# Kernel tuning notes

Hardware: AMD Instinct MI355X
Metric: run time of the kernel (lower is better)

## Reference

```python
import jax, jax.numpy as jnp
import numpy as np

DIM = 4096
N_HEADS = 32
N_KV = 8
HEAD_DIM = DIM // N_HEADS  # 128
R = N_HEADS // N_KV        # 4 query heads per kv head
B, T = 2, 2048


def setup_inputs() -> dict:
    key = jax.random.key(0)
    kx, kq, kkv, ko = jax.random.split(key, 4)
    scale = 0.02
    return {
        "x": jax.random.normal(kx, (B, T, DIM), dtype=jnp.float32),
        "Wq": jax.random.normal(kq, (DIM, DIM), dtype=jnp.float32) * scale,
        "Wkv": jax.random.normal(kkv, (2 * N_KV * HEAD_DIM, DIM), dtype=jnp.float32) * scale,
        "Wo": jax.random.normal(ko, (DIM, DIM), dtype=jnp.float32) * scale,
    }


def reference(x, Wq, Wkv, Wo):
    Bs, Ts, C = x.shape
    # projections (torch Linear: y = x @ W.T)
    q = (x @ Wq.T).reshape(Bs, Ts, N_HEADS, HEAD_DIM).transpose(0, 2, 1, 3)  # [B,H,T,hd]
    kv = x @ Wkv.T                                                            # [B,T,2*KV*hd]
    k, v = jnp.split(kv, 2, axis=-1)
    k = k.reshape(Bs, Ts, N_KV, HEAD_DIM).transpose(0, 2, 1, 3)  # [B,KV,T,hd]
    v = v.reshape(Bs, Ts, N_KV, HEAD_DIM).transpose(0, 2, 1, 3)  # [B,KV,T,hd]
    # grouped query heads: head h = g*R + r matches repeat_interleave(R, dim=1)
    qg = q.reshape(Bs, N_KV, R, Ts, HEAD_DIM)                    # [B,KV,R,T,hd]
    inv_scale = 1.0 / np.sqrt(HEAD_DIM).astype(np.float32)
    scores = jnp.einsum("bgrtd,bgsd->bgrts", qg, k) * inv_scale  # [B,KV,R,T,T]
    causal = jnp.tril(jnp.ones((Ts, Ts), dtype=bool))
    scores = jnp.where(causal, scores, jnp.finfo(scores.dtype).min)
    attn = jax.nn.softmax(scores, axis=-1)
    o = jnp.einsum("bgrts,bgsd->bgrtd", attn, v)                 # [B,KV,R,T,hd]
    o = o.reshape(Bs, N_HEADS, Ts, HEAD_DIM).transpose(0, 2, 1, 3).reshape(Bs, Ts, C)
    return o @ Wo.T
```

## Files before the change

### kernel.cpp

```cpp
#include <hip/hip_runtime.h>
#include <hip/hip_bf16.h>
#include <cstdint>
#include <type_traits>

#define DIM    4096
#define NHEADS 32
#define NKVH   8
#define HD     128
#define BATCH  2
#define SEQ    2048
#define MROWS  (BATCH*SEQ)
#define NQKV   6144
#define KOFF   4096
#define VOFF   5120

typedef __attribute__((ext_vector_type(8))) __bf16 bf16x8;
typedef __attribute__((ext_vector_type(4))) __bf16 bf16x4;
typedef __attribute__((ext_vector_type(4))) float  f32x4;

#define QSCALE 0.1275174338f

__device__ __forceinline__ void gl_lds16(const __bf16* g, __bf16* l) {
    __builtin_amdgcn_global_load_lds(
        (const __attribute__((address_space(1))) void*)g,
        (__attribute__((address_space(3))) void*)l, 16, 0, 0);
}

__global__ void cast_f32_bf16(const float* __restrict__ s, __bf16* __restrict__ d, int n8) {
    int i = blockIdx.x * 256 + threadIdx.x;
    if (i >= n8) return;
    float4 a = ((const float4*)s)[2*i];
    float4 b = ((const float4*)s)[2*i+1];
    bf16x8 v;
    v[0]=(__bf16)a.x; v[1]=(__bf16)a.y; v[2]=(__bf16)a.z; v[3]=(__bf16)a.w;
    v[4]=(__bf16)b.x; v[5]=(__bf16)b.y; v[6]=(__bf16)b.z; v[7]=(__bf16)b.w;
    ((bf16x8*)d)[i] = v;
}

template<typename OutT>
__global__ __launch_bounds__(256)
void gemm_bt(const __bf16* __restrict__ A, const __bf16* __restrict__ Bm,
             OutT* __restrict__ C, int M, int N, int K,
             float scale, int scale_cols)
{
    __shared__ __bf16 As[128*64];
    __shared__ __bf16 Bs[128*64];
    const int tid  = threadIdx.x;
    const int lane = tid & 63;
    const int w    = tid >> 6;
    const int quad = lane >> 4;
    const int l16  = lane & 15;
    const int m0   = blockIdx.y * 128;
    const int n0   = blockIdx.x * 128;
    const int wm   = (w & 1) * 64;
    const int wn   = (w >> 1) * 64;

    const __bf16* Ab = A  + (size_t)m0 * K;
    const __bf16* Bb = Bm + (size_t)n0 * K;

    f32x4 acc[4][4] = {};

    for (int k0 = 0; k0 < K; k0 += 64) {
        __syncthreads();
        #pragma unroll
        for (int r = 0; r < 4; ++r) {
            int chunk = r*256 + tid;
            int row = chunk >> 3, c8 = chunk & 7;
            int c8s = c8 ^ (row & 7);
            gl_lds16(Ab + (size_t)row*K + k0 + c8s*8, As + chunk*8);
            gl_lds16(Bb + (size_t)row*K + k0 + c8s*8, Bs + chunk*8);
        }
        __syncthreads();
        #pragma unroll
        for (int t = 0; t < 2; ++t) {
            bf16x8 af[4], bfr[4];
            #pragma unroll
            for (int i = 0; i < 4; ++i) {
                int row = wm + i*16 + l16;
                int cc  = (t*4 + quad) ^ (row & 7);
                af[i] = *(const bf16x8*)(As + row*64 + cc*8);
            }
            #pragma unroll
            for (int j = 0; j < 4; ++j) {
                int row = wn + j*16 + l16;
                int cc  = (t*4 + quad) ^ (row & 7);
                bfr[j] = *(const bf16x8*)(Bs + row*64 + cc*8);
            }
            #pragma unroll
            for (int i = 0; i < 4; ++i)
                #pragma unroll
                for (int j = 0; j < 4; ++j)
                    acc[i][j] = __builtin_amdgcn_mfma_f32_16x16x32_bf16(af[i], bfr[j], acc[i][j], 0,0,0);
        }
    }

    #pragma unroll
    for (int i = 0; i < 4; ++i) {
        #pragma unroll
        for (int j = 0; j < 4; ++j) {
            int col = n0 + wn + j*16 + l16;
            float sc = (col < scale_cols) ? scale : 1.0f;
            #pragma unroll
            for (int r = 0; r < 4; ++r) {
                int row = m0 + wm + i*16 + quad*4 + r;
                float v = acc[i][j][r] * sc;
                if constexpr (std::is_same<OutT, float>::value)
                    C[(size_t)row * N + col] = v;
                else
                    C[(size_t)row * N + col] = (__bf16)v;
            }
        }
    }
}

__global__ void transpose_v(const __bf16* __restrict__ qkv, __bf16* __restrict__ vt) {
    int idx  = blockIdx.x * 256 + threadIdx.x;
    int s8   = idx & 255;
    int rest = idx >> 8;
    int d    = rest & (HD-1);
    int bg   = rest >> 7;
    int b    = bg >> 3;
    int g    = bg & 7;
    int s0   = s8 * 8;
    const __bf16* src = qkv + (size_t)(b*SEQ + s0)*NQKV + VOFF + g*HD + d;
    bf16x8 v;
    #pragma unroll
    for (int u = 0; u < 8; ++u) v[u] = src[(size_t)u*NQKV];
    *(bf16x8*)(vt + (size_t)rest*SEQ + s0) = v;
}

__global__ __launch_bounds__(256, 4)
void flash_attn(const __bf16* __restrict__ qkv, const __bf16* __restrict__ vt,
                __bf16* __restrict__ O)
{
    __shared__ __bf16 Ks[64*128];
    __shared__ __bf16 Vts[128*64];
    __shared__ __bf16 Ps[64*64];

    const int qt = (gridDim.x - 1) - blockIdx.x;
    const int bh = blockIdx.y;
    const int b  = bh >> 5;
    const int h  = bh & 31;
    const int g  = h >> 2;
    const int q0 = qt * 64;

    const int tid  = threadIdx.x;
    const int lane = tid & 63;
    const int w    = tid >> 6;
    const int quad = lane >> 4;
    const int l16  = lane & 15;
    const int psw  = (l16 & 7) << 1;

    const __bf16* Qb  = qkv + (size_t)(b*SEQ + q0)*NQKV + h*HD;
    const __bf16* Kb  = qkv + (size_t)(b*SEQ)*NQKV + KOFF + g*HD;
    const __bf16* Vtb = vt  + (size_t)((b*NKVH + g)*HD)*SEQ;

    bf16x8 qf[4];
    #pragma unroll
    for (int t = 0; t < 4; ++t)
        qf[t] = *(const bf16x8*)(Qb + (size_t)(w*16 + l16)*NQKV + t*32 + quad*8);

    f32x4 o_acc[8] = {};
    float m_i = -1e30f, l_i = 0.f;
    const int myrow = q0 + w*16 + l16;

    const int nkt = qt + 1;
    for (int kt = 0; kt < nkt; ++kt) {
        const int s0 = kt * 64;
        __syncthreads();
        #pragma unroll
        for (int r = 0; r < 4; ++r) {
            int c = r*256 + tid;
            { int row = c >> 4, c16 = c & 15;
              int c16s = c16 ^ (row & 7);
              gl_lds16(Kb + (size_t)(s0 + row)*NQKV + c16s*8, Ks + c*8); }
            { int dd = c >> 3, c8 = c & 7;
              int c8s = c8 ^ (dd & 7);
              gl_lds16(Vtb + (size_t)dd*SEQ + s0 + c8s*8, Vts + c*8); }
        }
        __syncthreads();

        f32x4 s_acc[4] = {};
        #pragma unroll
        for (int t = 0; t < 4; ++t) {
            #pragma unroll
            for (int j = 0; j < 4; ++j) {
                int row = j*16 + l16;
                int cc  = (t*4 + quad) ^ (row & 7);
                bf16x8 bk = *(const bf16x8*)(Ks + row*128 + cc*8);
                s_acc[j] = __builtin_amdgcn_mfma_f32_16x16x32_bf16(bk, qf[t], s_acc[j], 0,0,0);
            }
        }

        if (kt == nkt - 1) {
            #pragma unroll
            for (int j = 0; j < 4; ++j)
                #pragma unroll
                for (int r = 0; r < 4; ++r)
                    if (s0 + j*16 + quad*4 + r > myrow) s_acc[j][r] = -1e30f;
        }

        float pm = s_acc[0][0];
        #pragma unroll
        for (int j = 0; j < 4; ++j)
            #pragma unroll
            for (int r = 0; r < 4; ++r)
                pm = fmaxf(pm, s_acc[j][r]);
        pm = fmaxf(pm, __shfl_xor(pm, 16));
        pm = fmaxf(pm, __shfl_xor(pm, 32));
        float mnew  = fmaxf(m_i, pm);
        float alpha = exp2f(m_i - mnew);
        m_i = mnew;

        float psum = 0.f;
        #pragma unroll
        for (int j = 0; j < 4; ++j) {
            bf16x4 pv;
            #pragma unroll
            for (int r = 0; r < 4; ++r) {
                float p = exp2f(s_acc[j][r] - mnew);
                psum += p;
                pv[r] = (__bf16)p;
            }
            int cs = (j*4 + quad) ^ psw;
            *(bf16x4*)(Ps + (w*16 + l16)*64 + cs*4) = pv;
        }
        psum += __shfl_xor(psum, 16);
        psum += __shfl_xor(psum, 32);
        l_i = l_i*alpha + psum;

        float av[4];
        #pragma unroll
        for (int r = 0; r < 4; ++r) av[r] = __shfl(alpha, quad*4 + r);
        #pragma unroll
        for (int jt = 0; jt < 8; ++jt)
            #pragma unroll
            for (int r = 0; r < 4; ++r)
                o_acc[jt][r] *= av[r];

        #pragma unroll
        for (int t = 0; t < 2; ++t) {
            int cs = (t*8 + quad*2) ^ psw;
            bf16x8 ap = *(const bf16x8*)(Ps + (w*16 + l16)*64 + cs*4);
            #pragma unroll
            for (int jt = 0; jt < 8; ++jt) {
                int row = jt*16 + l16;
                int cc  = (t*4 + quad) ^ (row & 7);
                bf16x8 bv = *(const bf16x8*)(Vts + row*64 + cc*8);
                o_acc[jt] = __builtin_amdgcn_mfma_f32_16x16x32_bf16(ap, bv, o_acc[jt], 0,0,0);
            }
        }
    }

    float inv = 1.0f / l_i;
    float ivr[4];
    #pragma unroll
    for (int r = 0; r < 4; ++r) ivr[r] = __shfl(inv, quad*4 + r);
    #pragma unroll
    for (int jt = 0; jt < 8; ++jt) {
        #pragma unroll
        for (int r = 0; r < 4; ++r) {
            int row = q0 + w*16 + quad*4 + r;
            int col = h*HD + jt*16 + l16;
            O[(size_t)(b*SEQ + row)*DIM + col] = (__bf16)(o_acc[jt][r] * ivr[r]);
        }
    }
}

extern "C" void kernel_launch(void* const* d_in, const int* in_sizes, int n_in,
                              void* d_out, int out_size, void* d_ws, size_t ws_size,
                              hipStream_t stream) {
    const float* x   = (const float*)d_in[0];
    const float* Wq  = (const float*)d_in[1];
    const float* Wkv = (const float*)d_in[2];
    const float* Wo  = (const float*)d_in[3];

    const size_t OFF_XB   = 0;
    const size_t OFF_WQKV = 33554432;
    const size_t OFF_WO   = 83886080;
    const size_t OFF_QKV  = 117440512;
    const size_t OFF_VT   = 167772160;
    const size_t OFF_OB   = 176160768;
    const size_t NEEDED   = 209715200;
    if (ws_size < NEEDED) return;

    char* ws = (char*)d_ws;
    __bf16* xb   = (__bf16*)(ws + OFF_XB);
    __bf16* wqkv = (__bf16*)(ws + OFF_WQKV);
    __bf16* wo   = (__bf16*)(ws + OFF_WO);
    __bf16* qkv  = (__bf16*)(ws + OFF_QKV);
    __bf16* vt   = (__bf16*)(ws + OFF_VT);
    __bf16* ob   = (__bf16*)(ws + OFF_OB);

    cast_f32_bf16<<<16777216/8/256, 256, 0, stream>>>(x,   xb,              16777216/8);
    cast_f32_bf16<<<16777216/8/256, 256, 0, stream>>>(Wq,  wqkv,            16777216/8);
    cast_f32_bf16<<< 8388608/8/256, 256, 0, stream>>>(Wkv, wqkv + 16777216,  8388608/8);
    cast_f32_bf16<<<16777216/8/256, 256, 0, stream>>>(Wo,  wo,              16777216/8);

    gemm_bt<__bf16><<<dim3(NQKV/128, MROWS/128), 256, 0, stream>>>(
        xb, wqkv, qkv, MROWS, NQKV, DIM, QSCALE, DIM);

    transpose_v<<<524288/256, 256, 0, stream>>>(qkv, vt);

    flash_attn<<<dim3(SEQ/64, BATCH*NHEADS), 256, 0, stream>>>(qkv, vt, ob);

    gemm_bt<float><<<dim3(DIM/128, MROWS/128), 256, 0, stream>>>(
        ob, wo, (float*)d_out, MROWS, DIM, DIM, 1.0f, 0);
}
```

Baseline: 864.9 us.

## Double-buffer K/V tiles and enlarge flash-attention query tile to 128 rows

The flash attention kernel now processes 128 query rows per block with 512 threads (8 waves) and double-buffers the K and V^T shared-memory tiles. The next tile's async global-to-LDS load is issued before computing on the current one, with a single barrier per iteration. Waves skip key tiles that lie entirely above their causal diagonal, and masking runs only on tiles that straddle it. Each K/V tile is reused across twice as many query rows, and global-load latency is meant to overlap with MFMA work. The cost is higher LDS use (about 80KB per block) and fewer blocks, which may lower occupancy, and waves with skipped tiles sit idle at the barriers.

```diff
diff --git a/kernel.cpp b/kernel.cpp
--- a/kernel.cpp
+++ b/kernel.cpp
@@ -129,20 +129,20 @@
     *(bf16x8*)(vt + (size_t)rest*SEQ + s0) = v;
 }
 
-__global__ __launch_bounds__(256, 4)
+__global__ __launch_bounds__(512, 4)
 void flash_attn(const __bf16* __restrict__ qkv, const __bf16* __restrict__ vt,
                 __bf16* __restrict__ O)
 {
-    __shared__ __bf16 Ks[64*128];
-    __shared__ __bf16 Vts[128*64];
-    __shared__ __bf16 Ps[64*64];
+    __shared__ __bf16 Ks[2][64*128];
+    __shared__ __bf16 Vts[2][128*64];
+    __shared__ __bf16 Ps[128*64];
 
     const int qt = (gridDim.x - 1) - blockIdx.x;
     const int bh = blockIdx.y;
     const int b  = bh >> 5;
     const int h  = bh & 31;
     const int g  = h >> 2;
-    const int q0 = qt * 64;
+    const int q0 = qt * 128;
 
     const int tid  = threadIdx.x;
     const int lane = tid & 63;
@@ -163,93 +163,120 @@
     f32x4 o_acc[8] = {};
     float m_i = -1e30f, l_i = 0.f;
     const int myrow = q0 + w*16 + l16;
-
-    const int nkt = qt + 1;
+    const int wmin  = q0 + w*16;
+
+    const int nkt = 2*qt + 2;
+
+    #pragma unroll
+    for (int r = 0; r < 2; ++r) {
+        int c = r*512 + tid;
+        { int row = c >> 4, c16 = c & 15;
+          int c16s = c16 ^ (row & 7);
+          gl_lds16(Kb + (size_t)row*NQKV + c16s*8, &Ks[0][0] + c*8); }
+        { int dd = c >> 3, c8 = c & 7;
+          int c8s = c8 ^ (dd & 7);
+          gl_lds16(Vtb + (size_t)dd*SEQ + c8s*8, &Vts[0][0] + c*8); }
+    }
+    __syncthreads();
+
+    int cur = 0;
     for (int kt = 0; kt < nkt; ++kt) {
         const int s0 = kt * 64;
+
+        if (kt + 1 < nkt) {
+            const int sn = s0 + 64;
+            __bf16* Ksb  = &Ks[cur^1][0];
+            __bf16* Vtsb = &Vts[cur^1][0];
+            #pragma unroll
+            for (int r = 0; r < 2; ++r) {
+                int c = r*512 + tid;
+                { int row = c >> 4, c16 = c & 15;
+                  int c16s = c16 ^ (row & 7);
+                  gl_lds16(Kb + (size_t)(sn + row)*NQKV + c16s*8, Ksb + c*8); }
+                { int dd = c >> 3, c8 = c & 7;
+                  int c8s = c8 ^ (dd & 7);
+                  gl_lds16(Vtb + (size_t)dd*SEQ + sn + c8s*8, Vtsb + c*8); }
+            }
+        }
+
+        if (s0 <= wmin + 15) {
+            const __bf16* Ksb  = &Ks[cur][0];
+            const __bf16* Vtsb = &Vts[cur][0];
+
+            f32x4 s_acc[4] = {};
+            #pragma unroll
+            for (int t = 0; t < 4; ++t) {
+                #pragma unroll
+                for (int j = 0; j < 4; ++j) {
+                    int row = j*16 + l16;
+                    int cc  = (t*4 + quad) ^ (row & 7);
+                    bf16x8 bk = *(const bf16x8*)(Ksb + row*128 + cc*8);
+                    s_acc[j] = __builtin_amdgcn_mfma_f32_16x16x32_bf16(bk, qf[t], s_acc[j], 0,0,0);
+                }
+            }
+
+            if (s0 + 63 > wmin) {
+                #pragma unroll
+                for (int j = 0; j < 4; ++j)
+                    #pragma unroll
+                    for (int r = 0; r < 4; ++r)
+                        if (s0 + j*16 + quad*4 + r > myrow) s_acc[j][r] = -1e30f;
+            }
+
+            float pm = s_acc[0][0];
+            #pragma unroll
+            for (int j = 0; j < 4; ++j)
+                #pragma unroll
+                for (int r = 0; r < 4; ++r)
+                    pm = fmaxf(pm, s_acc[j][r]);
+            pm = fmaxf(pm, __shfl_xor(pm, 16));
+            pm = fmaxf(pm, __shfl_xor(pm, 32));
+            float mnew  = fmaxf(m_i, pm);
+            float alpha = exp2f(m_i - mnew);
+            m_i = mnew;
+
+            float psum = 0.f;
+            #pragma unroll
+            for (int j = 0; j < 4; ++j) {
+                bf16x4 pv;
+                #pragma unroll
+                for (int r = 0; r < 4; ++r) {
+                    float p = exp2f(s_acc[j][r] - mnew);
+                    psum += p;
+                    pv[r] = (__bf16)p;
+                }
+                int cs = (j*4 + quad) ^ psw;
+                *(bf16x4*)(Ps + (w*16 + l16)*64 + cs*4) = pv;
+            }
+            psum += __shfl_xor(psum, 16);
+            psum += __shfl_xor(psum, 32);
+            l_i = l_i*alpha + psum;
+
+            float av[4];
+            #pragma unroll
+            for (int r = 0; r < 4; ++r) av[r] = __shfl(alpha, quad*4 + r);
+            #pragma unroll
+            for (int jt = 0; jt < 8; ++jt)
+                #pragma unroll
+                for (int r = 0; r < 4; ++r)
+                    o_acc[jt][r] *= av[r];
+
+            #pragma unroll
+            for (int t = 0; t < 2; ++t) {
+                int cs = (t*8 + quad*2) ^ psw;
+                bf16x8 ap = *(const bf16x8*)(Ps + (w*16 + l16)*64 + cs*4);
+                #pragma unroll
+                for (int jt = 0; jt < 8; ++jt) {
+                    int row = jt*16 + l16;
+                    int cc  = (t*4 + quad) ^ (row & 7);
+                    bf16x8 bv = *(const bf16x8*)(Vtsb + row*64 + cc*8);
+                    o_acc[jt] = __builtin_amdgcn_mfma_f32_16x16x32_bf16(ap, bv, o_acc[jt], 0,0,0);
+                }
+            }
+        }
+
         __syncthreads();
-        #pragma unroll
-        for (int r = 0; r < 4; ++r) {
-            int c = r*256 + tid;
-            { int row = c >> 4, c16 = c & 15;
-              int c16s = c16 ^ (row & 7);
-              gl_lds16(Kb + (size_t)(s0 + row)*NQKV + c16s*8, Ks + c*8); }
-            { int dd = c >> 3, c8 = c & 7;
-              int c8s = c8 ^ (dd & 7);
-              gl_lds16(Vtb + (size_t)dd*SEQ + s0 + c8s*8, Vts + c*8); }
-        }
-        __syncthreads();
-
-        f32x4 s_acc[4] = {};
-        #pragma unroll
-        for (int t = 0; t < 4; ++t) {
-            #pragma unroll
-            for (int j = 0; j < 4; ++j) {
-                int row = j*16 + l16;
-                int cc  = (t*4 + quad) ^ (row & 7);
-                bf16x8 bk = *(const bf16x8*)(Ks + row*128 + cc*8);
-                s_acc[j] = __builtin_amdgcn_mfma_f32_16x16x32_bf16(bk, qf[t], s_acc[j], 0,0,0);
-            }
-        }
-
-        if (kt == nkt - 1) {
-            #pragma unroll
-            for (int j = 0; j < 4; ++j)
-                #pragma unroll
-                for (int r = 0; r < 4; ++r)
-                    if (s0 + j*16 + quad*4 + r > myrow) s_acc[j][r] = -1e30f;
-        }
-
-        float pm = s_acc[0][0];
-        #pragma unroll
-        for (int j = 0; j < 4; ++j)
-            #pragma unroll
-            for (int r = 0; r < 4; ++r)
-                pm = fmaxf(pm, s_acc[j][r]);
-        pm = fmaxf(pm, __shfl_xor(pm, 16));
-        pm = fmaxf(pm, __shfl_xor(pm, 32));
-        float mnew  = fmaxf(m_i, pm);
-        float alpha = exp2f(m_i - mnew);
-        m_i = mnew;
-
-        float psum = 0.f;
-        #pragma unroll
-        for (int j = 0; j < 4; ++j) {
-            bf16x4 pv;
-            #pragma unroll
-            for (int r = 0; r < 4; ++r) {
-                float p = exp2f(s_acc[j][r] - mnew);
-                psum += p;
-                pv[r] = (__bf16)p;
-            }
-            int cs = (j*4 + quad) ^ psw;
-            *(bf16x4*)(Ps + (w*16 + l16)*64 + cs*4) = pv;
-        }
-        psum += __shfl_xor(psum, 16);
-        psum += __shfl_xor(psum, 32);
-        l_i = l_i*alpha + psum;
-
-        float av[4];
-        #pragma unroll
-        for (int r = 0; r < 4; ++r) av[r] = __shfl(alpha, quad*4 + r);
-        #pragma unroll
-        for (int jt = 0; jt < 8; ++jt)
-            #pragma unroll
-            for (int r = 0; r < 4; ++r)
-                o_acc[jt][r] *= av[r];
-
-        #pragma unroll
-        for (int t = 0; t < 2; ++t) {
-            int cs = (t*8 + quad*2) ^ psw;
-            bf16x8 ap = *(const bf16x8*)(Ps + (w*16 + l16)*64 + cs*4);
-            #pragma unroll
-            for (int jt = 0; jt < 8; ++jt) {
-                int row = jt*16 + l16;
-                int cc  = (t*4 + quad) ^ (row & 7);
-                bf16x8 bv = *(const bf16x8*)(Vts + row*64 + cc*8);
-                o_acc[jt] = __builtin_amdgcn_mfma_f32_16x16x32_bf16(ap, bv, o_acc[jt], 0,0,0);
-            }
-        }
+        cur ^= 1;
     }
 
     float inv = 1.0f / l_i;
@@ -302,7 +329,7 @@
 
     transpose_v<<<524288/256, 256, 0, stream>>>(qkv, vt);
 
-    flash_attn<<<dim3(SEQ/64, BATCH*NHEADS), 256, 0, stream>>>(qkv, vt, ob);
+    flash_attn<<<dim3(SEQ/128, BATCH*NHEADS), 512, 0, stream>>>(qkv, vt, ob);
 
     gemm_bt<float><<<dim3(DIM/128, MROWS/128), 256, 0, stream>>>(
         ob, wo, (float*)d_out, MROWS, DIM, DIM, 1.0f, 0);
```

Result: faster. 817.2 us (-5.5%).
